# Performance work log

Measured on AMD Instinct MI355X. Metric: run time of the kernel, lower is better.

Reference implementation:

```python
import jax, jax.numpy as jnp
import numpy as np
from jax import lax

B, IMG, CIN, C, HEADS, K = 2, 112, 64, 256, 8, 3  # kernel_size[0]=3 used by hatt1
HD = C // HEADS


def layer_norm(x, w, b, eps=1e-5):
    mu = jnp.mean(x, axis=-1, keepdims=True)
    var = jnp.mean((x - mu) ** 2, axis=-1, keepdims=True)
    return (x - mu) / jnp.sqrt(var + eps) * w + b


def conv3x3(x, w, b):
    # x: (B,Cin,H,W), w: (Cout,Cin,3,3) -- stride 1, pad 1 (OverlapPatchEmbed patchsize=3)
    y = lax.conv_general_dilated(x, w, (1, 1), ((1, 1), (1, 1)),
                                 dimension_numbers=('NCHW', 'OIHW', 'NCHW'))
    return y + b[None, :, None, None]


def nat_cross_attention(q_in, kv_in, wq, bq, wkv, bkv, rpb, wp, bp, heads=HEADS, k=K):
    # NATTEN-style 2D neighborhood attention with separate query / key-value maps.
    Bb, H, W, Cc = q_in.shape
    hd = Cc // heads
    scale = hd ** -0.5
    q = (q_in @ wq + bq).reshape(Bb, H, W, heads, hd) * scale
    kv = (kv_in @ wkv + bkv).reshape(Bb, H, W, 2, heads, hd)
    kk, v = kv[:, :, :, 0], kv[:, :, :, 1]
    half = k // 2
    # border-clamped window starts -> every pixel attends to a full k x k window
    si = jnp.clip(jnp.arange(H) - half, 0, H - k)  # (H,)
    sj = jnp.clip(jnp.arange(W) - half, 0, W - k)  # (W,)
    nbi = si[:, None] + jnp.arange(k)  # (H,k) neighbor rows
    nbj = sj[:, None] + jnp.arange(k)  # (W,k) neighbor cols

    def gather(t):  # t: (B,H,W,heads,hd) -> (B,H,W,heads,k*k,hd)
        g = t[:, nbi]            # (B,H,k,W,heads,hd)
        g = g[:, :, :, nbj]      # (B,H,k,W,k,heads,hd)
        return jnp.transpose(g, (0, 1, 3, 5, 2, 4, 6)).reshape(Bb, H, W, heads, k * k, hd)

    kg, vg = gather(kk), gather(v)
    logits = jnp.einsum('bijhd,bijhnd->bijhn', q, kg)
    # relative position bias: rpb (heads, 2k-1, 2k-1)
    pi = jnp.arange(H) - si  # query position inside its window, 0..k-1
    pj = jnp.arange(W) - sj
    idx_i = jnp.arange(k)[None, :] - pi[:, None] + (k - 1)  # (H,k) in [0, 2k-2]
    idx_j = jnp.arange(k)[None, :] - pj[:, None] + (k - 1)  # (W,k)
    bias = rpb[:, idx_i]           # (heads,H,k,2k-1)
    bias = bias[:, :, :, idx_j]    # (heads,H,k,W,k)
    bias = jnp.transpose(bias, (1, 3, 0, 2, 4)).reshape(H, W, heads, k * k)
    attn = jax.nn.softmax(logits + bias, axis=-1)
    out = jnp.einsum('bijhn,bijhnd->bijhd', attn, vg).reshape(Bb, H, W, Cc)
    return out @ wp + bp


def setup_inputs() -> dict:
    key = jax.random.key(0)
    ks = jax.random.split(key, 24)
    std = 0.02
    inp = {
        'xq': jax.random.normal(ks[0], (B, CIN, IMG, IMG), jnp.float32),
        'xkv': jax.random.normal(ks[1], (B, CIN, IMG, IMG), jnp.float32),
        'conv1_w': jax.random.normal(ks[2], (C, CIN, 3, 3), jnp.float32) * std,
        'conv1_b': jnp.zeros((C,), jnp.float32),
        'conv3_w': jax.random.normal(ks[3], (C, CIN, 3, 3), jnp.float32) * std,
        'conv3_b': jnp.zeros((C,), jnp.float32),
        'ln1_w': jnp.ones((C,), jnp.float32), 'ln1_b': jnp.zeros((C,), jnp.float32),
        'ln10_w': jnp.ones((C,), jnp.float32), 'ln10_b': jnp.zeros((C,), jnp.float32),
        'ln3_w': jnp.ones((C,), jnp.float32), 'ln3_b': jnp.zeros((C,), jnp.float32),
        'wq': jax.random.normal(ks[4], (C, C), jnp.float32) * std,
        'bq': jnp.zeros((C,), jnp.float32),
        'wkv': jax.random.normal(ks[5], (C, 2 * C), jnp.float32) * std,
        'bkv': jnp.zeros((2 * C,), jnp.float32),
        'rpb': jax.random.normal(ks[6], (HEADS, 2 * K - 1, 2 * K - 1), jnp.float32) * std,
        'wp': jax.random.normal(ks[7], (C, C), jnp.float32) * std,
        'bp': jnp.zeros((C,), jnp.float32),
        'fc1_w': jax.random.normal(ks[8], (C, 2 * C), jnp.float32) * std,
        'fc1_b': jnp.zeros((2 * C,), jnp.float32),
        'fc2_w': jax.random.normal(ks[9], (2 * C, C), jnp.float32) * std,
        'fc2_b': jnp.zeros((C,), jnp.float32),
    }
    return inp


def reference(xq, xkv, conv1_w, conv1_b, conv3_w, conv3_b, ln1_w, ln1_b, ln10_w, ln10_b,
              ln3_w, ln3_b, wq, bq, wkv, bkv, rpb, wp, bp, fc1_w, fc1_b, fc2_w, fc2_b):
    # patch embeds (stride-1 3x3 conv, pad 1), channels-last maps (B,H,W,C)
    x1 = jnp.transpose(conv3x3(xq, conv1_w, conv1_b), (0, 2, 3, 1))
    x3 = jnp.transpose(conv3x3(xkv, conv3_w, conv3_b), (0, 2, 3, 1))
    qn = layer_norm(x1, ln1_w, ln1_b)    # norm1(x_embedding1)
    kvn = layer_norm(x1, ln10_w, ln10_b)  # norm1_0(x_embedding1)
    att1 = nat_cross_attention(qn, kvn, wq, bq, wkv, bkv, rpb, wp, bp)
    att = att1 + x3  # drop_path is identity at inference
    h = layer_norm(att, ln3_w, ln3_b)
    m = jax.nn.gelu(h @ fc1_w + fc1_b, approximate=False) @ fc2_w + fc2_b
    x = m + att
    return jnp.transpose(x, (0, 3, 1, 2))  # (B,C,H,W)
```

## Files before the change

### kernel.cpp

```cpp
#include <hip/hip_runtime.h>
#include <math.h>

#define IMG 112
#define CIN 64
#define CH 256
#define PADW 114
#define IMG2 12544
#define NPIX 25088
#define SCQ 0.17677669529663687f

typedef __bf16 bf16;
typedef __bf16 bf16x8 __attribute__((ext_vector_type(8)));
typedef float f32x4 __attribute__((ext_vector_type(4)));

__device__ __forceinline__ void gld_lds16(const void* g, void* l) {
    __builtin_amdgcn_global_load_lds(
        (const __attribute__((address_space(1))) void*)g,
        (__attribute__((address_space(3))) void*)l,
        16, 0, 0);
}
#define VMCNT0() asm volatile("s_waitcnt vmcnt(0)" ::: "memory")
#define BAR() __builtin_amdgcn_s_barrier()

__global__ __launch_bounds__(256) void prep_kernel(
    const float* __restrict__ xq, const float* __restrict__ xkv,
    bf16* __restrict__ padq, bf16* __restrict__ padkv,
    const float* __restrict__ c1w, const float* __restrict__ c3w,
    bf16* __restrict__ cw1, bf16* __restrict__ cw2,
    const float* __restrict__ wq, bf16* __restrict__ wqt,
    const float* __restrict__ wkv, bf16* __restrict__ wkvt,
    const float* __restrict__ wp, bf16* __restrict__ wpt,
    const float* __restrict__ f1w, bf16* __restrict__ wf1,
    const float* __restrict__ f2w, bf16* __restrict__ wf2) {
    int bid = blockIdx.x, tid = threadIdx.x;
    __shared__ float lds[CIN * 113];
    if (bid < 448) {
        const float* in = (bid < 224) ? xq : xkv;
        bf16* out = (bid < 224) ? padq : padkv;
        int bi = (bid < 224) ? bid : bid - 224;
        int b = bi / IMG, i = bi % IMG;
        const float* src = in + (size_t)b * CIN * IMG2 + (size_t)i * IMG;
        for (int t = tid; t < CIN * IMG; t += 256) {
            int ci = t / IMG, j = t - ci * IMG;
            lds[ci * 113 + j] = src[(size_t)ci * IMG2 + j];
        }
        __syncthreads();
        bf16* dst = out + (((size_t)(b * PADW + (i + 1)) * PADW) + 1) * CIN;
        for (int t = tid; t < CIN * IMG; t += 256) {
            int j = t / CIN, ci = t - j * CIN;
            dst[(size_t)j * CIN + ci] = (bf16)lds[ci * 113 + j];
        }
        bf16* rowbase = out + ((size_t)(b * PADW + (i + 1)) * PADW) * CIN;
        if (tid < 128) rowbase[(tid >> 6 ? 113 * CIN : 0) + (tid & 63)] = (bf16)0.0f;
        if (i == 0)
            for (int t = tid; t < PADW * CIN; t += 256)
                out[((size_t)(b * PADW + 0) * PADW) * CIN + t] = (bf16)0.0f;
        if (i == IMG - 1)
            for (int t = tid; t < PADW * CIN; t += 256)
                out[((size_t)(b * PADW + 113) * PADW) * CIN + t] = (bf16)0.0f;
    } else if (bid < 1024) {
        int idx = (bid - 448) * 256 + tid;
        int co = idx / 576, r = idx - co * 576;
        int tap = r >> 6, ci = r & 63;
        int src = co * 576 + ci * 9 + tap;
        cw1[idx] = (bf16)c1w[src];
        cw2[idx] = (bf16)c3w[src];
    } else {
        int off = (bid - 1024) * 256 + tid;
        const float* in; bf16* out; int K, N; float sc = 1.0f; int base;
        if (off < 65536)       { in = wq;  out = wqt;  K = 256; N = 256; sc = SCQ; base = 0; }
        else if (off < 196608) { in = wkv; out = wkvt; K = 256; N = 512; base = 65536; }
        else if (off < 262144) { in = wp;  out = wpt;  K = 256; N = 256; base = 196608; }
        else if (off < 393216) { in = f1w; out = wf1;  K = 256; N = 512; base = 262144; }
        else                   { in = f2w; out = wf2;  K = 512; N = 256; base = 393216; }
        int idx = off - base;
        int n = idx / K, k = idx - n * K;
        out[idx] = (bf16)(in[(size_t)k * N + n] * sc);
    }
}

#define M_DENSE 0
#define M_LN2   1
#define M_WPLN  2
#define M_GELU  3
#define M_NCHW  4
#define TS 264
#define TFS 258

template <int AMODE, int MODE>
__device__ __forceinline__ void gemm_core(
    char* sm,
    const bf16* __restrict__ A, const bf16* __restrict__ B,
    const float* __restrict__ bias, float bscale,
    const bf16* __restrict__ res,
    bf16* __restrict__ out0, int ldo0,
    bf16* __restrict__ out1, float* __restrict__ outf,
    const float* __restrict__ lnw0, const float* __restrict__ lnb0,
    const float* __restrict__ lnw1, const float* __restrict__ lnb1,
    int K) {
    bf16* As = (bf16*)sm;
    bf16* Bs = (bf16*)(sm + 8192);
    float* lnb = (float*)sm;
    bf16* Tb = (bf16*)(sm + 2048);
    float* Tf = (float*)(sm + 2048);

    const int tid = threadIdx.x;
    const int wave = tid >> 6, lane = tid & 63;
    const int m0 = blockIdx.x * 64;
    const int wm = wave >> 1, wn = wave & 1;
    const int fr = lane & 15, fq = lane >> 4;
    const int srow = lane >> 3;
    const int scol = ((lane & 7) ^ srow) * 8;

    const bf16* aptr[2];
#pragma unroll
    for (int q = 0; q < 2; ++q) {
        int arow = m0 + wave * 16 + q * 8 + srow;
        if (AMODE == 1) {
            int b = arow / IMG2;
            int rem = arow - b * IMG2;
            int i = rem / IMG, j = rem - i * IMG;
            aptr[q] = A + ((size_t)((b * PADW + i) * PADW + j)) * CIN + scol;
        } else {
            aptr[q] = A + (size_t)arow * K + scol;
        }
    }
    const bf16* bptr0 = B + (size_t)(wave * 64 + srow) * K + scol;

    auto STAGE = [&](int kt) {
        int aoff = (AMODE == 1) ? ((kt / 3) * PADW + (kt - (kt / 3) * 3)) * CIN : kt * 64;
        int boff = kt * 64;
        bf16* ad = As + (wave * 16) * 64;
        gld_lds16(aptr[0] + aoff, ad);
        gld_lds16(aptr[1] + aoff, ad + 8 * 64);
        bf16* bd = Bs + (wave * 64) * 64;
#pragma unroll
        for (int u = 0; u < 8; ++u)
            gld_lds16(bptr0 + (size_t)u * 8 * K + boff, bd + u * 8 * 64);
    };

    f32x4 acc[2][8] = {};
    auto COMPUTE = [&]() {
#pragma unroll
        for (int ks = 0; ks < 2; ++ks) {
            int ch = ((ks * 4 + fq) ^ (fr & 7)) * 8;
            bf16x8 af[2];
#pragma unroll
            for (int mi = 0; mi < 2; ++mi) af[mi] = *(const bf16x8*)&As[(wm * 32 + mi * 16 + fr) * 64 + ch];
            bf16x8 bv[8];
#pragma unroll
            for (int ni = 0; ni < 8; ++ni) bv[ni] = *(const bf16x8*)&Bs[(wn * 128 + ni * 16 + fr) * 64 + ch];
#pragma unroll
            for (int mi = 0; mi < 2; ++mi)
#pragma unroll
                for (int ni = 0; ni < 8; ++ni)
                    acc[mi][ni] = __builtin_amdgcn_mfma_f32_16x16x32_bf16(af[mi], bv[ni], acc[mi][ni], 0, 0, 0);
        }
    };

    const int nk = K >> 6;
    for (int kt = 0; kt < nk; ++kt) {
        STAGE(kt);
        VMCNT0();
        BAR();
        COMPUTE();
        BAR();
    }

    float bvv[8];
#pragma unroll
    for (int ni = 0; ni < 8; ++ni) bvv[ni] = bias[wn * 128 + ni * 16 + fr] * bscale;
#pragma unroll
    for (int mi = 0; mi < 2; ++mi)
#pragma unroll
        for (int ni = 0; ni < 8; ++ni)
#pragma unroll
            for (int r = 0; r < 4; ++r) {
                float x = acc[mi][ni][r] + bvv[ni];
                if (MODE == M_WPLN) {
                    int prow = m0 + wm * 32 + mi * 16 + fq * 4 + r;
                    int col = wn * 128 + ni * 16 + fr;
                    x += (float)res[(size_t)prow * 256 + col];
                }
                if (MODE == M_GELU) x = 0.5f * x * (1.0f + erff(x * 0.70710678118f));
                acc[mi][ni][r] = x;
            }

    float mean_[2][4], rstd_[2][4];
    if (MODE == M_LN2 || MODE == M_WPLN) {
#pragma unroll
        for (int mi = 0; mi < 2; ++mi)
#pragma unroll
            for (int r = 0; r < 4; ++r) {
                float s = 0.0f, ss = 0.0f;
#pragma unroll
                for (int ni = 0; ni < 8; ++ni) {
                    float x = acc[mi][ni][r];
                    s += x; ss += x * x;
                }
#pragma unroll
                for (int msk = 1; msk <= 8; msk <<= 1) {
                    s += __shfl_xor(s, msk);
                    ss += __shfl_xor(ss, msk);
                }
                if (fr == 0) {
                    int row = wm * 32 + mi * 16 + fq * 4 + r;
                    lnb[wn * 128 + row] = s;
                    lnb[wn * 128 + 64 + row] = ss;
                }
            }
        BAR();
#pragma unroll
        for (int mi = 0; mi < 2; ++mi)
#pragma unroll
            for (int r = 0; r < 4; ++r) {
                int row = wm * 32 + mi * 16 + fq * 4 + r;
                float s = lnb[row] + lnb[128 + row];
                float ss = lnb[64 + row] + lnb[192 + row];
                float mean = s * (1.0f / CH);
                float var = ss * (1.0f / CH) - mean * mean;
                mean_[mi][r] = mean;
                rstd_[mi][r] = rsqrtf(var + 1e-5f);
            }
    }

    if (MODE == M_NCHW) {
        int c = tid;
        int b = m0 / IMG2, p0 = m0 - b * IMG2;
        float* outp = outf + ((size_t)(b * CH + c)) * IMG2 + p0;
        const bf16* rp = res + (size_t)m0 * 256 + c;
#pragma unroll
        for (int p = 0; p < 2; ++p) {
            if (wm == p) {
#pragma unroll
                for (int mi = 0; mi < 2; ++mi)
#pragma unroll
                    for (int ni = 0; ni < 8; ++ni)
#pragma unroll
                        for (int r = 0; r < 4; ++r)
                            Tf[(mi * 16 + fq * 4 + r) * TFS + wn * 128 + ni * 16 + fr] = acc[mi][ni][r];
            }
            BAR();
#pragma unroll
            for (int g = 0; g < 8; ++g) {
                f32x4 v;
#pragma unroll
                for (int e = 0; e < 4; ++e)
                    v[e] = Tf[(g * 4 + e) * TFS + c] + (float)rp[(size_t)(p * 32 + g * 4 + e) * 256];
                *(f32x4*)(outp + p * 32 + g * 4) = v;
            }
            BAR();
        }
    } else {
#pragma unroll
        for (int mi = 0; mi < 2; ++mi)
#pragma unroll
            for (int ni = 0; ni < 8; ++ni)
#pragma unroll
                for (int r = 0; r < 4; ++r) {
                    int row = wm * 32 + mi * 16 + fq * 4 + r;
                    int col = wn * 128 + ni * 16 + fr;
                    float x = acc[mi][ni][r];
                    if (MODE == M_LN2) x = (x - mean_[mi][r]) * rstd_[mi][r];
                    Tb[row * TS + (col ^ ((row & 7) << 3))] = (bf16)x;
                }
        BAR();
        int row = tid & 63, qd = tid >> 6;
        int cb = qd * 64;
        int xr = (row & 7) << 3;
        if (MODE == M_DENSE || MODE == M_GELU) {
            bf16* op = out0 + (size_t)(m0 + row) * ldo0 + cb;
#pragma unroll
            for (int g = 0; g < 8; ++g)
                *(bf16x8*)(op + g * 8) = *(const bf16x8*)&Tb[row * TS + ((cb + g * 8) ^ xr)];
        } else if (MODE == M_LN2) {
            bf16* op0 = out0 + (size_t)(m0 + row) * 256 + cb;
            bf16* op1 = out1 + (size_t)(m0 + row) * 256 + cb;
#pragma unroll
            for (int g = 0; g < 8; ++g) {
                bf16x8 xh = *(const bf16x8*)&Tb[row * TS + ((cb + g * 8) ^ xr)];
                bf16x8 o0, o1;
#pragma unroll
                for (int e = 0; e < 8; ++e) {
                    int c = cb + g * 8 + e;
                    float v = (float)xh[e];
                    o0[e] = (bf16)(v * lnw0[c] + lnb0[c]);
                    o1[e] = (bf16)(v * lnw1[c] + lnb1[c]);
                }
                *(bf16x8*)(op0 + g * 8) = o0;
                *(bf16x8*)(op1 + g * 8) = o1;
            }
        } else if (MODE == M_WPLN) {
            float s = lnb[row] + lnb[128 + row];
            float ss = lnb[64 + row] + lnb[192 + row];
            float mean = s * (1.0f / CH);
            float rstd = rsqrtf(ss * (1.0f / CH) - mean * mean + 1e-5f);
            bf16* op0 = out0 + (size_t)(m0 + row) * 256 + cb;
            bf16* op1 = out1 + (size_t)(m0 + row) * 256 + cb;
#pragma unroll
            for (int g = 0; g < 8; ++g) {
                bf16x8 xv = *(const bf16x8*)&Tb[row * TS + ((cb + g * 8) ^ xr)];
                bf16x8 o1;
#pragma unroll
                for (int e = 0; e < 8; ++e) {
                    int c = cb + g * 8 + e;
                    o1[e] = (bf16)(((float)xv[e] - mean) * rstd * lnw0[c] + lnb0[c]);
                }
                *(bf16x8*)(op0 + g * 8) = xv;
                *(bf16x8*)(op1 + g * 8) = o1;
            }
        }
    }
}

#define SMEMSZ 40960

__global__ __launch_bounds__(256, 3) void conv_kernel(
    const bf16* padq, const bf16* padkv, const bf16* cw1, const bf16* cw2,
    const float* c1b, const float* c3b,
    bf16* qn, bf16* kvn, bf16* x3,
    const float* l1w, const float* l1b, const float* l10w, const float* l10b) {
    __shared__ __align__(16) char sm[SMEMSZ];
    if (blockIdx.y == 0)
        gemm_core<1, M_LN2>(sm, padq, cw1, c1b, 1.0f, nullptr, qn, 256, kvn, nullptr,
                            l1w, l1b, l10w, l10b, 576);
    else
        gemm_core<1, M_DENSE>(sm, padkv, cw2, c3b, 1.0f, nullptr, x3, 256, nullptr, nullptr,
                              nullptr, nullptr, nullptr, nullptr, 576);
}

__global__ __launch_bounds__(256, 3) void qkv_kernel(
    const bf16* qnp, const bf16* kvnp, const bf16* wqt, const bf16* wkvt,
    const float* bq, const float* bkv, bf16* q, bf16* kv) {
    __shared__ __align__(16) char sm[SMEMSZ];
    int by = blockIdx.y;
    const bf16* A = by ? kvnp : qnp;
    const bf16* B = by ? (wkvt + (size_t)(by - 1) * 65536) : wqt;
    const float* bias = by ? (bkv + (by - 1) * 256) : bq;
    float bsc = by ? 1.0f : SCQ;
    bf16* out = by ? (kv + (by - 1) * 256) : q;
    int ldo = by ? 512 : 256;
    gemm_core<0, M_DENSE>(sm, A, B, bias, bsc, nullptr, out, ldo, nullptr, nullptr,
                          nullptr, nullptr, nullptr, nullptr, 256);
}

__global__ __launch_bounds__(256, 3) void wp_kernel(
    const bf16* ao, const bf16* wpt, const float* bp, const bf16* x3,
    bf16* att, bf16* h, const float* l3w, const float* l3b) {
    __shared__ __align__(16) char sm[SMEMSZ];
    gemm_core<0, M_WPLN>(sm, ao, wpt, bp, 1.0f, x3, att, 256, h, nullptr,
                         l3w, l3b, nullptr, nullptr, 256);
}

__global__ __launch_bounds__(256, 3) void fc1_kernel(
    const bf16* h, const bf16* wf1, const float* f1b, bf16* m1) {
    __shared__ __align__(16) char sm[SMEMSZ];
    int by = blockIdx.y;
    gemm_core<0, M_GELU>(sm, h, wf1 + (size_t)by * 65536, f1b + by * 256, 1.0f, nullptr,
                         m1 + by * 256, 512, nullptr, nullptr,
                         nullptr, nullptr, nullptr, nullptr, 256);
}

__global__ __launch_bounds__(256, 3) void fc2_kernel(
    const bf16* m1, const bf16* wf2, const float* f2b, const bf16* att, float* out) {
    __shared__ __align__(16) char sm[SMEMSZ];
    gemm_core<0, M_NCHW>(sm, m1, wf2, f2b, 1.0f, att, nullptr, 0, nullptr, out,
                         nullptr, nullptr, nullptr, nullptr, 512);
}

__global__ __launch_bounds__(256) void attn_kernel(const bf16* __restrict__ q, const bf16* __restrict__ kv,
                                                   const float* __restrict__ rpb, bf16* __restrict__ out) {
    int idx = blockIdx.x * 256 + threadIdx.x;
    int h = idx & 7, p = idx >> 3;
    int b = p / IMG2;
    int rem = p - b * IMG2;
    int i = rem / IMG, j = rem - i * IMG;
    int si = i - 1; if (si < 0) si = 0; if (si > IMG - 3) si = IMG - 3;
    int sj = j - 1; if (sj < 0) sj = 0; if (sj > IMG - 3) sj = IMG - 3;
    int pi = i - si, pj = j - sj;

    float qv[32];
    {
        const bf16x8* qp = (const bf16x8*)(q + (size_t)p * CH + h * 32);
#pragma unroll
        for (int g = 0; g < 4; ++g) {
            bf16x8 t = qp[g];
#pragma unroll
            for (int e = 0; e < 8; ++e) qv[g * 8 + e] = (float)t[e];
        }
    }
    float logits[9];
#pragma unroll
    for (int a = 0; a < 3; ++a) {
#pragma unroll
        for (int bb = 0; bb < 3; ++bb) {
            int pn = (b * IMG + (si + a)) * IMG + (sj + bb);
            const bf16x8* kp = (const bf16x8*)(kv + (size_t)pn * 512 + h * 32);
            float s = 0.0f;
#pragma unroll
            for (int g = 0; g < 4; ++g) {
                bf16x8 t = kp[g];
#pragma unroll
                for (int e = 0; e < 8; ++e) s += qv[g * 8 + e] * (float)t[e];
            }
            logits[a * 3 + bb] = s + rpb[(h * 5 + (a - pi + 2)) * 5 + (bb - pj + 2)];
        }
    }
    float mx = logits[0];
#pragma unroll
    for (int n = 1; n < 9; ++n) mx = fmaxf(mx, logits[n]);
    float den = 0.0f;
#pragma unroll
    for (int n = 0; n < 9; ++n) { logits[n] = expf(logits[n] - mx); den += logits[n]; }
    float inv = 1.0f / den;
    float o[32] = {};
#pragma unroll
    for (int a = 0; a < 3; ++a) {
#pragma unroll
        for (int bb = 0; bb < 3; ++bb) {
            int pn = (b * IMG + (si + a)) * IMG + (sj + bb);
            float wgt = logits[a * 3 + bb] * inv;
            const bf16x8* vp = (const bf16x8*)(kv + (size_t)pn * 512 + 256 + h * 32);
#pragma unroll
            for (int g = 0; g < 4; ++g) {
                bf16x8 t = vp[g];
#pragma unroll
                for (int e = 0; e < 8; ++e) o[g * 8 + e] += wgt * (float)t[e];
            }
        }
    }
    bf16* op = out + (size_t)p * CH + h * 32;
#pragma unroll
    for (int g = 0; g < 4; ++g) {
        bf16x8 t;
#pragma unroll
        for (int e = 0; e < 8; ++e) t[e] = (bf16)o[g * 8 + e];
        *(bf16x8*)(op + g * 8) = t;
    }
}

extern "C" void kernel_launch(void* const* d_in, const int* in_sizes, int n_in,
                              void* d_out, int out_size, void* d_ws, size_t ws_size,
                              hipStream_t stream) {
    (void)in_sizes; (void)n_in; (void)out_size; (void)ws_size;
    const float* xq    = (const float*)d_in[0];
    const float* xkv   = (const float*)d_in[1];
    const float* c1w   = (const float*)d_in[2];
    const float* c1b   = (const float*)d_in[3];
    const float* c3w   = (const float*)d_in[4];
    const float* c3b   = (const float*)d_in[5];
    const float* ln1w  = (const float*)d_in[6];
    const float* ln1b  = (const float*)d_in[7];
    const float* ln10w = (const float*)d_in[8];
    const float* ln10b = (const float*)d_in[9];
    const float* ln3w  = (const float*)d_in[10];
    const float* ln3b  = (const float*)d_in[11];
    const float* wq    = (const float*)d_in[12];
    const float* bq    = (const float*)d_in[13];
    const float* wkv   = (const float*)d_in[14];
    const float* bkv   = (const float*)d_in[15];
    const float* rpb   = (const float*)d_in[16];
    const float* wp    = (const float*)d_in[17];
    const float* bp    = (const float*)d_in[18];
    const float* f1w   = (const float*)d_in[19];
    const float* f1b   = (const float*)d_in[20];
    const float* f2w   = (const float*)d_in[21];
    const float* f2b   = (const float*)d_in[22];
    float* out = (float*)d_out;

    char* ws = (char*)d_ws;
    bf16* PADQ  = (bf16*)(ws + 0);
    bf16* PADKV = (bf16*)(ws + 3326976);
    bf16* CW1   = (bf16*)(ws + 6653952);
    bf16* CW2   = (bf16*)(ws + 6948864);
    bf16* WQT   = (bf16*)(ws + 7243776);
    bf16* WKVT  = (bf16*)(ws + 7374848);
    bf16* WPT   = (bf16*)(ws + 7636992);
    bf16* WF1   = (bf16*)(ws + 7768064);
    bf16* WF2   = (bf16*)(ws + 8030208);
    bf16* QN    = (bf16*)(ws + 8292352);
    bf16* KVN   = (bf16*)(ws + 21137408);
    bf16* Q     = (bf16*)(ws + 33982464);
    bf16* KV    = (bf16*)(ws + 46827520);
    bf16* AO    = (bf16*)(ws + 72517632);
    bf16* X3    = (bf16*)(ws + 85362688);
    bf16* ATT   = (bf16*)(ws + 98207744);
    bf16* H     = (bf16*)(ws + 111052800);
    bf16* M1    = (bf16*)(ws + 123897856);

    prep_kernel<<<3072, 256, 0, stream>>>(xq, xkv, PADQ, PADKV, c1w, c3w, CW1, CW2,
                                          wq, WQT, wkv, WKVT, wp, WPT, f1w, WF1, f2w, WF2);
    conv_kernel<<<dim3(392, 2), 256, 0, stream>>>(PADQ, PADKV, CW1, CW2, c1b, c3b,
                                                  QN, KVN, X3, ln1w, ln1b, ln10w, ln10b);
    qkv_kernel<<<dim3(392, 3), 256, 0, stream>>>(QN, KVN, WQT, WKVT, bq, bkv, Q, KV);
    attn_kernel<<<784, 256, 0, stream>>>(Q, KV, rpb, AO);
    wp_kernel<<<392, 256, 0, stream>>>(AO, WPT, bp, X3, ATT, H, ln3w, ln3b);
    fc1_kernel<<<dim3(392, 2), 256, 0, stream>>>(H, WF1, f1b, M1);
    fc2_kernel<<<392, 256, 0, stream>>>(M1, WF2, f2b, ATT, out);
}
```

Before: 305.2 us.

## Replace LDS-staged GEMM with direct global-to-register MFMA loads and 32-row tiles

The shared GEMM core no longer stages A and B tiles through LDS with global_load_lds and per-k barriers. Each wave now loads its MFMA fragments straight from global memory into registers, with a fully unrolled K loop fixed at compile time. The M tile shrinks from 64 to 32 rows and every GEMM launch doubles its grid. This removes barrier and LDS traffic and raises block count, but each weight fragment is now read from global/L2 by every block with no reuse across waves, and the loads have only 16-byte, partly strided coalescing.

```diff
diff --git a/kernel.cpp b/kernel.cpp
--- a/kernel.cpp
+++ b/kernel.cpp
@@ -12,15 +12,6 @@
 typedef __bf16 bf16;
 typedef __bf16 bf16x8 __attribute__((ext_vector_type(8)));
 typedef float f32x4 __attribute__((ext_vector_type(4)));
-
-__device__ __forceinline__ void gld_lds16(const void* g, void* l) {
-    __builtin_amdgcn_global_load_lds(
-        (const __attribute__((address_space(1))) void*)g,
-        (__attribute__((address_space(3))) void*)l,
-        16, 0, 0);
-}
-#define VMCNT0() asm volatile("s_waitcnt vmcnt(0)" ::: "memory")
-#define BAR() __builtin_amdgcn_s_barrier()
 
 __global__ __launch_bounds__(256) void prep_kernel(
     const float* __restrict__ xq, const float* __restrict__ xkv,
@@ -85,9 +76,9 @@
 #define M_GELU  3
 #define M_NCHW  4
 #define TS 264
-#define TFS 258
-
-template <int AMODE, int MODE>
+#define TFS 257
+
+template <int AMODE, int MODE, int KK>
 __device__ __forceinline__ void gemm_core(
     char* sm,
     const bf16* __restrict__ A, const bf16* __restrict__ B,
@@ -96,224 +87,174 @@
     bf16* __restrict__ out0, int ldo0,
     bf16* __restrict__ out1, float* __restrict__ outf,
     const float* __restrict__ lnw0, const float* __restrict__ lnb0,
-    const float* __restrict__ lnw1, const float* __restrict__ lnb1,
-    int K) {
-    bf16* As = (bf16*)sm;
-    bf16* Bs = (bf16*)(sm + 8192);
-    float* lnb = (float*)sm;
-    bf16* Tb = (bf16*)(sm + 2048);
-    float* Tf = (float*)(sm + 2048);
+    const float* __restrict__ lnw1, const float* __restrict__ lnb1) {
+    constexpr int NK = KK >> 6;
+    bf16* Tb = (bf16*)sm;
+    float* Tf = (float*)sm;
+    float* lnb = (float*)(sm + 33024);
 
     const int tid = threadIdx.x;
     const int wave = tid >> 6, lane = tid & 63;
-    const int m0 = blockIdx.x * 64;
     const int wm = wave >> 1, wn = wave & 1;
     const int fr = lane & 15, fq = lane >> 4;
-    const int srow = lane >> 3;
-    const int scol = ((lane & 7) ^ srow) * 8;
-
-    const bf16* aptr[2];
-#pragma unroll
-    for (int q = 0; q < 2; ++q) {
-        int arow = m0 + wave * 16 + q * 8 + srow;
+    const int m0 = blockIdx.x * 32;
+
+    const bf16* baseA;
+    {
+        int arow = m0 + wm * 16 + fr;
         if (AMODE == 1) {
             int b = arow / IMG2;
             int rem = arow - b * IMG2;
             int i = rem / IMG, j = rem - i * IMG;
-            aptr[q] = A + ((size_t)((b * PADW + i) * PADW + j)) * CIN + scol;
+            baseA = A + ((size_t)((b * PADW + i) * PADW + j)) * CIN + fq * 8;
         } else {
-            aptr[q] = A + (size_t)arow * K + scol;
-        }
-    }
-    const bf16* bptr0 = B + (size_t)(wave * 64 + srow) * K + scol;
-
-    auto STAGE = [&](int kt) {
-        int aoff = (AMODE == 1) ? ((kt / 3) * PADW + (kt - (kt / 3) * 3)) * CIN : kt * 64;
-        int boff = kt * 64;
-        bf16* ad = As + (wave * 16) * 64;
-        gld_lds16(aptr[0] + aoff, ad);
-        gld_lds16(aptr[1] + aoff, ad + 8 * 64);
-        bf16* bd = Bs + (wave * 64) * 64;
-#pragma unroll
-        for (int u = 0; u < 8; ++u)
-            gld_lds16(bptr0 + (size_t)u * 8 * K + boff, bd + u * 8 * 64);
-    };
-
-    f32x4 acc[2][8] = {};
-    auto COMPUTE = [&]() {
+            baseA = A + (size_t)arow * KK + fq * 8;
+        }
+    }
+    const bf16* baseB[8];
+#pragma unroll
+    for (int ni = 0; ni < 8; ++ni)
+        baseB[ni] = B + (size_t)(wn * 128 + ni * 16 + fr) * KK + fq * 8;
+
+    f32x4 acc[8] = {};
+#pragma unroll
+    for (int kt = 0; kt < NK; ++kt) {
+        const int aoff = (AMODE == 1) ? ((kt / 3) * PADW + (kt % 3)) * CIN : kt * 64;
 #pragma unroll
         for (int ks = 0; ks < 2; ++ks) {
-            int ch = ((ks * 4 + fq) ^ (fr & 7)) * 8;
-            bf16x8 af[2];
-#pragma unroll
-            for (int mi = 0; mi < 2; ++mi) af[mi] = *(const bf16x8*)&As[(wm * 32 + mi * 16 + fr) * 64 + ch];
+            bf16x8 av = *(const bf16x8*)(baseA + aoff + ks * 32);
             bf16x8 bv[8];
 #pragma unroll
-            for (int ni = 0; ni < 8; ++ni) bv[ni] = *(const bf16x8*)&Bs[(wn * 128 + ni * 16 + fr) * 64 + ch];
-#pragma unroll
-            for (int mi = 0; mi < 2; ++mi)
-#pragma unroll
-                for (int ni = 0; ni < 8; ++ni)
-                    acc[mi][ni] = __builtin_amdgcn_mfma_f32_16x16x32_bf16(af[mi], bv[ni], acc[mi][ni], 0, 0, 0);
-        }
-    };
-
-    const int nk = K >> 6;
-    for (int kt = 0; kt < nk; ++kt) {
-        STAGE(kt);
-        VMCNT0();
-        BAR();
-        COMPUTE();
-        BAR();
-    }
-
-    float bvv[8];
-#pragma unroll
-    for (int ni = 0; ni < 8; ++ni) bvv[ni] = bias[wn * 128 + ni * 16 + fr] * bscale;
-#pragma unroll
-    for (int mi = 0; mi < 2; ++mi)
-#pragma unroll
-        for (int ni = 0; ni < 8; ++ni)
+            for (int ni = 0; ni < 8; ++ni)
+                bv[ni] = *(const bf16x8*)(baseB[ni] + kt * 64 + ks * 32);
+#pragma unroll
+            for (int ni = 0; ni < 8; ++ni)
+                acc[ni] = __builtin_amdgcn_mfma_f32_16x16x32_bf16(av, bv[ni], acc[ni], 0, 0, 0);
+        }
+    }
+
+#pragma unroll
+    for (int ni = 0; ni < 8; ++ni) {
+        int col = wn * 128 + ni * 16 + fr;
+        float bv = bias[col] * bscale;
+#pragma unroll
+        for (int r = 0; r < 4; ++r) {
+            float x = acc[ni][r] + bv;
+            if (MODE == M_WPLN) {
+                int prow = m0 + wm * 16 + fq * 4 + r;
+                x += (float)res[(size_t)prow * 256 + col];
+            }
+            if (MODE == M_GELU) x = 0.5f * x * (1.0f + erff(x * 0.70710678118f));
+            acc[ni][r] = x;
+        }
+    }
+
+    const int rloc0 = wm * 16 + fq * 4;
+
+    if (MODE == M_LN2 || MODE == M_WPLN) {
+#pragma unroll
+        for (int r = 0; r < 4; ++r) {
+            float s = 0.0f, ss = 0.0f;
+#pragma unroll
+            for (int ni = 0; ni < 8; ++ni) {
+                float x = acc[ni][r];
+                s += x; ss += x * x;
+            }
+#pragma unroll
+            for (int msk = 1; msk <= 8; msk <<= 1) {
+                s += __shfl_xor(s, msk);
+                ss += __shfl_xor(ss, msk);
+            }
+            if (fr == 0) {
+                lnb[wn * 64 + rloc0 + r] = s;
+                lnb[wn * 64 + 32 + rloc0 + r] = ss;
+            }
+        }
+        __syncthreads();
+    }
+
+    if (MODE == M_NCHW) {
+#pragma unroll
+        for (int ni = 0; ni < 8; ++ni) {
+            int col = wn * 128 + ni * 16 + fr;
 #pragma unroll
             for (int r = 0; r < 4; ++r) {
-                float x = acc[mi][ni][r] + bvv[ni];
-                if (MODE == M_WPLN) {
-                    int prow = m0 + wm * 32 + mi * 16 + fq * 4 + r;
-                    int col = wn * 128 + ni * 16 + fr;
-                    x += (float)res[(size_t)prow * 256 + col];
+                int prow = m0 + rloc0 + r;
+                Tf[(rloc0 + r) * TFS + col] = acc[ni][r] + (float)res[(size_t)prow * 256 + col];
+            }
+        }
+        __syncthreads();
+        int b = m0 / IMG2, p0 = m0 - b * IMG2;
+#pragma unroll
+        for (int it = 0; it < 8; ++it) {
+            int ch = it * 32 + (tid >> 3);
+            int px = (tid & 7) * 4;
+            f32x4 v;
+#pragma unroll
+            for (int e = 0; e < 4; ++e) v[e] = Tf[(px + e) * TFS + ch];
+            *(f32x4*)(outf + ((size_t)(b * CH + ch)) * IMG2 + p0 + px) = v;
+        }
+    } else {
+        float mean_[4], rstd_[4];
+        if (MODE == M_LN2) {
+#pragma unroll
+            for (int r = 0; r < 4; ++r) {
+                float s = lnb[rloc0 + r] + lnb[64 + rloc0 + r];
+                float ss = lnb[32 + rloc0 + r] + lnb[96 + rloc0 + r];
+                float mean = s * (1.0f / CH);
+                mean_[r] = mean;
+                rstd_[r] = rsqrtf(ss * (1.0f / CH) - mean * mean + 1e-5f);
+            }
+        }
+#pragma unroll
+        for (int ni = 0; ni < 8; ++ni) {
+            int col = wn * 128 + ni * 16 + fr;
+#pragma unroll
+            for (int r = 0; r < 4; ++r) {
+                int row = rloc0 + r;
+                float x = acc[ni][r];
+                if (MODE == M_LN2) x = (x - mean_[r]) * rstd_[r];
+                Tb[row * TS + (col ^ ((row & 7) << 3))] = (bf16)x;
+            }
+        }
+        __syncthreads();
+#pragma unroll
+        for (int it = 0; it < 4; ++it) {
+            int row = it * 8 + (tid >> 5);
+            int col = (tid & 31) * 8;
+            bf16x8 v = *(const bf16x8*)&Tb[row * TS + (col ^ ((row & 7) << 3))];
+            if (MODE == M_DENSE || MODE == M_GELU) {
+                *(bf16x8*)(out0 + (size_t)(m0 + row) * ldo0 + col) = v;
+            } else if (MODE == M_LN2) {
+                bf16x8 o0, o1;
+#pragma unroll
+                for (int e = 0; e < 8; ++e) {
+                    int c = col + e;
+                    float xh = (float)v[e];
+                    o0[e] = (bf16)(xh * lnw0[c] + lnb0[c]);
+                    o1[e] = (bf16)(xh * lnw1[c] + lnb1[c]);
                 }
-                if (MODE == M_GELU) x = 0.5f * x * (1.0f + erff(x * 0.70710678118f));
-                acc[mi][ni][r] = x;
-            }
-
-    float mean_[2][4], rstd_[2][4];
-    if (MODE == M_LN2 || MODE == M_WPLN) {
-#pragma unroll
-        for (int mi = 0; mi < 2; ++mi)
-#pragma unroll
-            for (int r = 0; r < 4; ++r) {
-                float s = 0.0f, ss = 0.0f;
-#pragma unroll
-                for (int ni = 0; ni < 8; ++ni) {
-                    float x = acc[mi][ni][r];
-                    s += x; ss += x * x;
+                *(bf16x8*)(out0 + (size_t)(m0 + row) * 256 + col) = o0;
+                *(bf16x8*)(out1 + (size_t)(m0 + row) * 256 + col) = o1;
+            } else {
+                float s = lnb[row] + lnb[64 + row];
+                float ss = lnb[32 + row] + lnb[96 + row];
+                float mean = s * (1.0f / CH);
+                float rstd = rsqrtf(ss * (1.0f / CH) - mean * mean + 1e-5f);
+                bf16x8 o1;
+#pragma unroll
+                for (int e = 0; e < 8; ++e) {
+                    int c = col + e;
+                    o1[e] = (bf16)(((float)v[e] - mean) * rstd * lnw0[c] + lnb0[c]);
                 }
-#pragma unroll
-                for (int msk = 1; msk <= 8; msk <<= 1) {
-                    s += __shfl_xor(s, msk);
-                    ss += __shfl_xor(ss, msk);
-                }
-                if (fr == 0) {
-                    int row = wm * 32 + mi * 16 + fq * 4 + r;
-                    lnb[wn * 128 + row] = s;
-                    lnb[wn * 128 + 64 + row] = ss;
-                }
-            }
-        BAR();
-#pragma unroll
-        for (int mi = 0; mi < 2; ++mi)
-#pragma unroll
-            for (int r = 0; r < 4; ++r) {
-                int row = wm * 32 + mi * 16 + fq * 4 + r;
-                float s = lnb[row] + lnb[128 + row];
-                float ss = lnb[64 + row] + lnb[192 + row];
-                float mean = s * (1.0f / CH);
-                float var = ss * (1.0f / CH) - mean * mean;
-                mean_[mi][r] = mean;
-                rstd_[mi][r] = rsqrtf(var + 1e-5f);
-            }
-    }
-
-    if (MODE == M_NCHW) {
-        int c = tid;
-        int b = m0 / IMG2, p0 = m0 - b * IMG2;
-        float* outp = outf + ((size_t)(b * CH + c)) * IMG2 + p0;
-        const bf16* rp = res + (size_t)m0 * 256 + c;
-#pragma unroll
-        for (int p = 0; p < 2; ++p) {
-            if (wm == p) {
-#pragma unroll
-                for (int mi = 0; mi < 2; ++mi)
-#pragma unroll
-                    for (int ni = 0; ni < 8; ++ni)
-#pragma unroll
-                        for (int r = 0; r < 4; ++r)
-                            Tf[(mi * 16 + fq * 4 + r) * TFS + wn * 128 + ni * 16 + fr] = acc[mi][ni][r];
-            }
-            BAR();
-#pragma unroll
-            for (int g = 0; g < 8; ++g) {
-                f32x4 v;
-#pragma unroll
-                for (int e = 0; e < 4; ++e)
-                    v[e] = Tf[(g * 4 + e) * TFS + c] + (float)rp[(size_t)(p * 32 + g * 4 + e) * 256];
-                *(f32x4*)(outp + p * 32 + g * 4) = v;
-            }
-            BAR();
-        }
-    } else {
-#pragma unroll
-        for (int mi = 0; mi < 2; ++mi)
-#pragma unroll
-            for (int ni = 0; ni < 8; ++ni)
-#pragma unroll
-                for (int r = 0; r < 4; ++r) {
-                    int row = wm * 32 + mi * 16 + fq * 4 + r;
-                    int col = wn * 128 + ni * 16 + fr;
-                    float x = acc[mi][ni][r];
-                    if (MODE == M_LN2) x = (x - mean_[mi][r]) * rstd_[mi][r];
-                    Tb[row * TS + (col ^ ((row & 7) << 3))] = (bf16)x;
-                }
-        BAR();
-        int row = tid & 63, qd = tid >> 6;
-        int cb = qd * 64;
-        int xr = (row & 7) << 3;
-        if (MODE == M_DENSE || MODE == M_GELU) {
-            bf16* op = out0 + (size_t)(m0 + row) * ldo0 + cb;
-#pragma unroll
-            for (int g = 0; g < 8; ++g)
-                *(bf16x8*)(op + g * 8) = *(const bf16x8*)&Tb[row * TS + ((cb + g * 8) ^ xr)];
-        } else if (MODE == M_LN2) {
-            bf16* op0 = out0 + (size_t)(m0 + row) * 256 + cb;
-            bf16* op1 = out1 + (size_t)(m0 + row) * 256 + cb;
-#pragma unroll
-            for (int g = 0; g < 8; ++g) {
-                bf16x8 xh = *(const bf16x8*)&Tb[row * TS + ((cb + g * 8) ^ xr)];
-                bf16x8 o0, o1;
-#pragma unroll
-                for (int e = 0; e < 8; ++e) {
-                    int c = cb + g * 8 + e;
-                    float v = (float)xh[e];
-                    o0[e] = (bf16)(v * lnw0[c] + lnb0[c]);
-                    o1[e] = (bf16)(v * lnw1[c] + lnb1[c]);
-                }
-                *(bf16x8*)(op0 + g * 8) = o0;
-                *(bf16x8*)(op1 + g * 8) = o1;
-            }
-        } else if (MODE == M_WPLN) {
-            float s = lnb[row] + lnb[128 + row];
-            float ss = lnb[64 + row] + lnb[192 + row];
-            float mean = s * (1.0f / CH);
-            float rstd = rsqrtf(ss * (1.0f / CH) - mean * mean + 1e-5f);
-            bf16* op0 = out0 + (size_t)(m0 + row) * 256 + cb;
-            bf16* op1 = out1 + (size_t)(m0 + row) * 256 + cb;
-#pragma unroll
-            for (int g = 0; g < 8; ++g) {
-                bf16x8 xv = *(const bf16x8*)&Tb[row * TS + ((cb + g * 8) ^ xr)];
-                bf16x8 o1;
-#pragma unroll
-                for (int e = 0; e < 8; ++e) {
-                    int c = cb + g * 8 + e;
-                    o1[e] = (bf16)(((float)xv[e] - mean) * rstd * lnw0[c] + lnb0[c]);
-                }
-                *(bf16x8*)(op0 + g * 8) = xv;
-                *(bf16x8*)(op1 + g * 8) = o1;
-            }
-        }
-    }
-}
-
-#define SMEMSZ 40960
+                *(bf16x8*)(out0 + (size_t)(m0 + row) * 256 + col) = v;
+                *(bf16x8*)(out1 + (size_t)(m0 + row) * 256 + col) = o1;
+            }
+        }
+    }
+}
+
+#define SMEMSZ 34816
 
 __global__ __launch_bounds__(256, 3) void conv_kernel(
     const bf16* padq, const bf16* padkv, const bf16* cw1, const bf16* cw2,
@@ -322,11 +263,11 @@
     const float* l1w, const float* l1b, const float* l10w, const float* l10b) {
     __shared__ __align__(16) char sm[SMEMSZ];
     if (blockIdx.y == 0)
-        gemm_core<1, M_LN2>(sm, padq, cw1, c1b, 1.0f, nullptr, qn, 256, kvn, nullptr,
-                            l1w, l1b, l10w, l10b, 576);
+        gemm_core<1, M_LN2, 576>(sm, padq, cw1, c1b, 1.0f, nullptr, qn, 256, kvn, nullptr,
+                                 l1w, l1b, l10w, l10b);
     else
-        gemm_core<1, M_DENSE>(sm, padkv, cw2, c3b, 1.0f, nullptr, x3, 256, nullptr, nullptr,
-                              nullptr, nullptr, nullptr, nullptr, 576);
+        gemm_core<1, M_DENSE, 576>(sm, padkv, cw2, c3b, 1.0f, nullptr, x3, 256, nullptr, nullptr,
+                                   nullptr, nullptr, nullptr, nullptr);
 }
 
 __global__ __launch_bounds__(256, 3) void qkv_kernel(
@@ -340,32 +281,32 @@
     float bsc = by ? 1.0f : SCQ;
     bf16* out = by ? (kv + (by - 1) * 256) : q;
     int ldo = by ? 512 : 256;
-    gemm_core<0, M_DENSE>(sm, A, B, bias, bsc, nullptr, out, ldo, nullptr, nullptr,
-                          nullptr, nullptr, nullptr, nullptr, 256);
+    gemm_core<0, M_DENSE, 256>(sm, A, B, bias, bsc, nullptr, out, ldo, nullptr, nullptr,
+                               nullptr, nullptr, nullptr, nullptr);
 }
 
 __global__ __launch_bounds__(256, 3) void wp_kernel(
     const bf16* ao, const bf16* wpt, const float* bp, const bf16* x3,
     bf16* att, bf16* h, const float* l3w, const float* l3b) {
     __shared__ __align__(16) char sm[SMEMSZ];
-    gemm_core<0, M_WPLN>(sm, ao, wpt, bp, 1.0f, x3, att, 256, h, nullptr,
-                         l3w, l3b, nullptr, nullptr, 256);
+    gemm_core<0, M_WPLN, 256>(sm, ao, wpt, bp, 1.0f, x3, att, 256, h, nullptr,
+                              l3w, l3b, nullptr, nullptr);
 }
 
 __global__ __launch_bounds__(256, 3) void fc1_kernel(
     const bf16* h, const bf16* wf1, const float* f1b, bf16* m1) {
     __shared__ __align__(16) char sm[SMEMSZ];
     int by = blockIdx.y;
-    gemm_core<0, M_GELU>(sm, h, wf1 + (size_t)by * 65536, f1b + by * 256, 1.0f, nullptr,
-                         m1 + by * 256, 512, nullptr, nullptr,
-                         nullptr, nullptr, nullptr, nullptr, 256);
+    gemm_core<0, M_GELU, 256>(sm, h, wf1 + (size_t)by * 65536, f1b + by * 256, 1.0f, nullptr,
+                              m1 + by * 256, 512, nullptr, nullptr,
+                              nullptr, nullptr, nullptr, nullptr);
 }
 
 __global__ __launch_bounds__(256, 3) void fc2_kernel(
     const bf16* m1, const bf16* wf2, const float* f2b, const bf16* att, float* out) {
     __shared__ __align__(16) char sm[SMEMSZ];
-    gemm_core<0, M_NCHW>(sm, m1, wf2, f2b, 1.0f, att, nullptr, 0, nullptr, out,
-                         nullptr, nullptr, nullptr, nullptr, 512);
+    gemm_core<0, M_NCHW, 512>(sm, m1, wf2, f2b, 1.0f, att, nullptr, 0, nullptr, out,
+                              nullptr, nullptr, nullptr, nullptr);
 }
 
 __global__ __launch_bounds__(256) void attn_kernel(const bf16* __restrict__ q, const bf16* __restrict__ kv,
@@ -490,11 +431,11 @@
 
     prep_kernel<<<3072, 256, 0, stream>>>(xq, xkv, PADQ, PADKV, c1w, c3w, CW1, CW2,
                                           wq, WQT, wkv, WKVT, wp, WPT, f1w, WF1, f2w, WF2);
-    conv_kernel<<<dim3(392, 2), 256, 0, stream>>>(PADQ, PADKV, CW1, CW2, c1b, c3b,
+    conv_kernel<<<dim3(784, 2), 256, 0, stream>>>(PADQ, PADKV, CW1, CW2, c1b, c3b,
                                                   QN, KVN, X3, ln1w, ln1b, ln10w, ln10b);
-    qkv_kernel<<<dim3(392, 3), 256, 0, stream>>>(QN, KVN, WQT, WKVT, bq, bkv, Q, KV);
+    qkv_kernel<<<dim3(784, 3), 256, 0, stream>>>(QN, KVN, WQT, WKVT, bq, bkv, Q, KV);
     attn_kernel<<<784, 256, 0, stream>>>(Q, KV, rpb, AO);
-    wp_kernel<<<392, 256, 0, stream>>>(AO, WPT, bp, X3, ATT, H, ln3w, ln3b);
-    fc1_kernel<<<dim3(392, 2), 256, 0, stream>>>(H, WF1, f1b, M1);
-    fc2_kernel<<<392, 256, 0, stream>>>(M1, WF2, f2b, ATT, out);
-}
+    wp_kernel<<<784, 256, 0, stream>>>(AO, WPT, bp, X3, ATT, H, ln3w, ln3b);
+    fc1_kernel<<<dim3(784, 2), 256, 0, stream>>>(H, WF1, f1b, M1);
+    fc2_kernel<<<784, 256, 0, stream>>>(M1, WF2, f2b, ATT, out);
+}
```

Result: slower. 521.5 us (+70.9%).
